# Performance work log

Hardware: AMD Instinct MI355X
Metric: run time of the kernel (lower is better)

The kernel has to match this reference:

```python
import jax, jax.numpy as jnp
import numpy as np

B, LS, LW, LV, M, D, H = 256, 1024, 1024, 1024, 16, 5120, 2048

def setup_inputs() -> dict:
    key = jax.random.key(0)
    ks = jax.random.split(key, 8)
    return {
        'phi_batch': jax.random.normal(ks[0], (B, LS), jnp.float32),
        'w_M_real': jax.random.normal(ks[1], (B, LW, M), jnp.float32),
        'w_M_imag': jax.random.normal(ks[2], (B, LW, M), jnp.float32),
        'v_M': jax.random.normal(ks[3], (LV, M), jnp.float32),
        'W1e': jax.random.normal(ks[4], (D, H), jnp.float32) * 0.02,
        'b1e': jnp.zeros((H,), jnp.float32),
        'W2e': jax.random.normal(ks[5], (H, LS), jnp.float32) * 0.02,
        'b2e': jnp.zeros((LS,), jnp.float32),
        'W1r': jax.random.normal(ks[6], (D, H), jnp.float32) * 0.02,
        'b1r': jnp.zeros((H,), jnp.float32),
        'W2r': jax.random.normal(ks[7], (H, 1), jnp.float32) * 0.02,
        'b2r': jnp.zeros((1,), jnp.float32),
    }

def reference(phi_batch, w_M_real, w_M_imag, v_M, W1e, b1e, W2e, b2e, W1r, b1r, W2r, b2r):
    b, ls = phi_batch.shape
    m = v_M.shape[1]
    # s = (1/sqrt(Ls)) * exp(1j*phi); use real/imag parts directly
    mag = 1.0 / jnp.sqrt(jnp.asarray(ls, jnp.float32))
    s_feat = jnp.concatenate([mag * jnp.cos(phi_batch), mag * jnp.sin(phi_batch)], axis=-1)  # [B, 2Ls]
    # Batched concat across (batch, M): replaces the nested Python loops
    X = jnp.concatenate([
        jnp.broadcast_to(s_feat[:, None, :], (b, m, s_feat.shape[-1])),
        jnp.swapaxes(w_M_real, 1, 2),                       # [B, M, Lw]
        jnp.swapaxes(w_M_imag, 1, 2),                       # [B, M, Lw]
        jnp.broadcast_to(v_M.T[None, :, :], (b, m, v_M.shape[0])),
    ], axis=-1)                                             # [B, M, D]
    eta_M = jax.nn.relu(X @ W1e + b1e) @ W2e + b2e          # [B, M, Ls]
    rho_M = (jax.nn.relu(X @ W1r + b1r) @ W2r + b2r)[..., 0]  # [B, M]
    eta = jnp.einsum('bm,bml->bl', rho_M, eta_M)            # sum_m rho_m * eta_m
    phi_optimal = phi_batch - eta
    return phi_optimal, jnp.swapaxes(eta_M, 1, 2)           # [B, Ls], [B, Ls, M]
```

## Files before the change

kernel.cpp:

```cpp
#include <hip/hip_runtime.h>
#include <hip/hip_bf16.h>
#include <stdint.h>

#define B_    256
#define LS_   1024
#define LW_   1024
#define LV_   1024
#define M_    16
#define D_    5120
#define H_    2048
#define ROWS  4096
#define N1    4096
#define KW    2048

typedef __hip_bfloat16 bf16;
typedef __bf16 bf16x8 __attribute__((ext_vector_type(8)));
typedef __bf16 bf16x4 __attribute__((ext_vector_type(4)));
typedef float f32x4 __attribute__((ext_vector_type(4)));

#define SB0() __builtin_amdgcn_sched_barrier(0)
#define LGKM(n) asm volatile("s_waitcnt lgkmcnt(" #n ")" ::: "memory")
#define VMC(n)  asm volatile("s_waitcnt vmcnt(" #n ")" ::: "memory")

__device__ __forceinline__ void gld_lds16(const void* g, void* l) {
  auto gp = (const __attribute__((address_space(1))) uint32_t*)(uintptr_t)g;
  auto lp = (__attribute__((address_space(3))) uint32_t*)(uint32_t)(uintptr_t)l;
  __builtin_amdgcn_global_load_lds(gp, lp, 16, 0, 0);
}

__device__ __forceinline__ void transpose64_body(char* sm, const float* __restrict__ in,
                                                 bf16* __restrict__ out,
                                                 int C, int R, int r0, int c0, int t) {
  float (*tile)[65] = (float (*)[65])sm;
  const int tx = t & 15, ty = t >> 4;
#pragma unroll
  for (int i = 0; i < 4; ++i) {
    const float4 v = *(const float4*)&in[(size_t)(r0 + ty + i * 16) * C + c0 + tx * 4];
    tile[ty + i * 16][tx * 4 + 0] = v.x;
    tile[ty + i * 16][tx * 4 + 1] = v.y;
    tile[ty + i * 16][tx * 4 + 2] = v.z;
    tile[ty + i * 16][tx * 4 + 3] = v.w;
  }
  __syncthreads();
#pragma unroll
  for (int i = 0; i < 4; ++i) {
    const int n = c0 + ty + i * 16;
    bf16x4 o;
#pragma unroll
    for (int j = 0; j < 4; ++j) o[j] = (__bf16)tile[tx * 4 + j][ty + i * 16];
    *(bf16x4*)&out[(size_t)n * R + r0 + tx * 4] = o;
  }
}

__global__ void __launch_bounds__(256)
prep_kernel(const float* __restrict__ phi,
            const float* __restrict__ wMr, const float* __restrict__ wMi,
            const float* __restrict__ vM,
            const float* __restrict__ W1e, const float* __restrict__ W1r,
            const float* __restrict__ W2e,
            bf16* __restrict__ sfeat, bf16* __restrict__ Awr,
            bf16* __restrict__ W1sT, bf16* __restrict__ W1wT,
            bf16* __restrict__ W2t, float* __restrict__ hVT) {
  __shared__ __align__(16) char sm[32768];
  const int bid = blockIdx.x;
  const int t = threadIdx.x;

  if (bid < 256) {
    float (*vs)[16] = (float (*)[16])sm;
    float (*ws)[16] = (float (*)[16])(sm + 16384);
    const float* Wb = (bid < 128) ? W1e : W1r;
    const int nbase = (bid & 127) * 16;
    const int nout = ((bid < 128) ? 0 : 2048) + nbase;
    const int m = t & 15, nl = t >> 4;
    float acc = 0.f;
    for (int l0 = 0; l0 < 1024; l0 += 256) {
      __syncthreads();
#pragma unroll
      for (int i = 0; i < 16; ++i) {
        int e = i * 256 + t, l = e >> 4, n = e & 15;
        vs[l][n] = vM[(size_t)(l0 + l) * 16 + n];
        ws[l][n] = Wb[(size_t)(4096 + l0 + l) * 2048 + nbase + n];
      }
      __syncthreads();
#pragma unroll 8
      for (int ll = 0; ll < 256; ++ll)
        acc += vs[ll][m] * ws[ll][nl];
    }
    hVT[(size_t)(nout + nl) * 16 + m] = acc;
  } else if (bid < 4352) {
    const int idx = bid - 256;
    const int z = idx >> 10, rem = idx & 1023;
    const float* src = (z == 0 || z == 2) ? W1e : W1r;
    src += (z < 2) ? 0 : (size_t)2048 * 2048;
    bf16* dst = (z < 2) ? W1sT : W1wT;
    dst += (z == 0 || z == 2) ? 0 : (size_t)2048 * 2048;
    transpose64_body(sm, src, dst, 2048, 2048, (rem >> 5) * 64, (rem & 31) * 64, t);
  } else if (bid < 4864) {
    const int idx = bid - 4352;
    transpose64_body(sm, W2e, W2t, LS_, H_, (idx >> 4) * 64, (idx & 15) * 64, t);
  } else if (bid < 8960) {
    const int idx = bid - 4864;
    const int b = idx >> 4, l0 = (idx & 15) * 64;
    float (*tr)[17] = (float (*)[17])sm;
    float (*ti)[17] = (float (*)[17])(sm + 4352 * 4);
    const float* wrb = wMr + (size_t)b * (LW_ * M_) + (size_t)l0 * 16;
    const float* wib = wMi + (size_t)b * (LW_ * M_) + (size_t)l0 * 16;
#pragma unroll
    for (int i = 0; i < 4; ++i) {
      int e = i * 256 + t, l = e >> 4, m = e & 15;
      tr[l][m] = wrb[e];
      ti[l][m] = wib[e];
    }
    __syncthreads();
    int m = t >> 4, t4 = t & 15;
    bf16* outR = Awr + (size_t)(b * 16 + m) * KW + l0;
#pragma unroll
    for (int j = 0; j < 4; ++j) outR[t4 * 4 + j]        = __float2bfloat16(tr[t4 * 4 + j][m]);
#pragma unroll
    for (int j = 0; j < 4; ++j) outR[1024 + t4 * 4 + j] = __float2bfloat16(ti[t4 * 4 + j][m]);
  } else {
    const int i = (bid - 8960) * 256 + t;
    const int b = i >> 10, l = i & 1023;
    float p = phi[i];
    float s, c;
    sincosf(p, &s, &c);
    sfeat[b * 2048 + l]        = __float2bfloat16(0.03125f * c);
    sfeat[b * 2048 + 1024 + l] = __float2bfloat16(0.03125f * s);
  }
}

__global__ void __launch_bounds__(256)
hsum_kernel(const float* __restrict__ hSp, const float* __restrict__ b1e,
            const float* __restrict__ b1r, float* __restrict__ hS2) {
  const int i = (blockIdx.x * 256 + threadIdx.x) * 4;
  const int c = i & (N1 - 1);
  f32x4 v = *(const f32x4*)&hSp[i];
  v = v + *(const f32x4*)&hSp[(size_t)B_ * N1 + i];
  v = v + *(const f32x4*)&hSp[(size_t)2 * B_ * N1 + i];
  v = v + *(const f32x4*)&hSp[(size_t)3 * B_ * N1 + i];
  const float* bp = (c < H_) ? &b1e[c] : &b1r[c - H_];
  v = v + *(const f32x4*)bp;
  *(f32x4*)&hS2[i] = v;
}

__global__ void __launch_bounds__(512, 2)
gemm1_256_kernel(const bf16* __restrict__ A, const bf16* __restrict__ Bt,
                 const float* __restrict__ hS2, const float* __restrict__ hVT,
                 const float* __restrict__ w2r,
                 bf16* __restrict__ outH, float* __restrict__ rhoP) {
  extern __shared__ __align__(16) char smem[];
  constexpr int NT = KW / 32;

  const int tid  = threadIdx.x;
  const int lane = tid & 63;
  const int wave = tid >> 6;
  const int wr = wave >> 2, wc = wave & 3;
  const int fr = lane & 15, fq = lane >> 4;
  const int row0 = blockIdx.y * 256, col0 = blockIdx.x * 256;

  const int slotF = (((fr & 1) << 2) | fq) ^ ((fr >> 1) & 7);
  const int aOff = (wr << 13) + ((fr >> 1) << 7) + (slotF << 4);
  const int bOff = 16384 + (wc << 12) + ((fr >> 1) << 7) + (slotF << 4);

  const int lg0 = (tid >> 3), lg1 = 64 + (tid >> 3);
  const int su0 = (tid & 7) ^ (lg0 & 7), su1 = (tid & 7) ^ (lg1 & 7);
  const int rowp0 = lg0 * 2 + (su0 >> 2), rowp1 = lg1 * 2 + (su1 >> 2);
  const int kb0 = (su0 & 3) << 4, kb1 = (su1 & 3) << 4;
  const char* pA0 = (const char*)A  + (size_t)(row0 + rowp0) * (KW * 2) + kb0;
  const char* pA1 = (const char*)A  + (size_t)(row0 + rowp1) * (KW * 2) + kb1;
  const char* pB0 = (const char*)Bt + (size_t)(col0 + rowp0) * (KW * 2) + kb0;
  const char* pB1 = (const char*)Bt + (size_t)(col0 + rowp1) * (KW * 2) + kb1;

  auto stageTile = [&](int T) {
    char* dst = smem + (size_t)(T & 3) * 32768;
    const size_t ko = (size_t)T * 64;
    gld_lds16(pA0 + ko, dst + 0     + tid * 16);
    gld_lds16(pA1 + ko, dst + 8192  + tid * 16);
    gld_lds16(pB0 + ko, dst + 16384 + tid * 16);
    gld_lds16(pB1 + ko, dst + 24576 + tid * 16);
  };

  f32x4 acc[8][4] = {};
  bf16x8 bA[4], bB[4];

  stageTile(0); stageTile(1); stageTile(2);
  VMC(4);
  __builtin_amdgcn_s_barrier();
  {
    const char* bP = smem + bOff;
#pragma unroll
    for (int n = 0; n < 4; ++n) bA[n] = *(const bf16x8*)(bP + n * 1024);
  }
  SB0();

  auto doIter = [&](int T, bf16x8 (&bCur)[4], bf16x8 (&bNxt)[4]) {
    const char* aP = smem + (size_t)(T & 3) * 32768 + aOff;
    const char* bP = smem + (size_t)((T + 1) & 3) * 32768 + bOff;
    bf16x8 a[8];
#pragma unroll
    for (int m = 0; m < 4; ++m) a[m] = *(const bf16x8*)(aP + m * 1024);
    SB0();
#pragma unroll
    for (int m = 4; m < 8; ++m) a[m] = *(const bf16x8*)(aP + m * 1024);
    SB0();
#pragma unroll
    for (int n = 0; n < 4; ++n) bNxt[n] = *(const bf16x8*)(bP + n * 1024);
    SB0();
    if (T + 3 < NT) stageTile(T + 3);
    SB0();
    LGKM(8);
    SB0();
    __builtin_amdgcn_s_setprio(1);
#pragma unroll
    for (int m = 0; m < 4; ++m)
#pragma unroll
      for (int n = 0; n < 4; ++n)
        acc[m][n] = __builtin_amdgcn_mfma_f32_16x16x32_bf16(a[m], bCur[n], acc[m][n], 0, 0, 0);
    SB0();
    LGKM(4);
    SB0();
#pragma unroll
    for (int m = 4; m < 8; ++m)
#pragma unroll
      for (int n = 0; n < 4; ++n)
        acc[m][n] = __builtin_amdgcn_mfma_f32_16x16x32_bf16(a[m], bCur[n], acc[m][n], 0, 0, 0);
    __builtin_amdgcn_s_setprio(0);
    SB0();
    LGKM(0);
    if (T + 3 < NT) { VMC(4); }
    else            { VMC(0); }
    __builtin_amdgcn_s_barrier();
  };

  for (int t = 0; t < NT - 2; t += 2) {
    doIter(t,     bA, bB);
    doIter(t + 1, bB, bA);
  }
  doIter(NT - 2, bA, bB);

  {
    const char* aP = smem + (size_t)((NT - 1) & 3) * 32768 + aOff;
    bf16x8 a[8];
#pragma unroll
    for (int m = 0; m < 4; ++m) a[m] = *(const bf16x8*)(aP + m * 1024);
    SB0();
#pragma unroll
    for (int m = 4; m < 8; ++m) a[m] = *(const bf16x8*)(aP + m * 1024);
    SB0();
    LGKM(4);
    SB0();
    __builtin_amdgcn_s_setprio(1);
#pragma unroll
    for (int m = 0; m < 4; ++m)
#pragma unroll
      for (int n = 0; n < 4; ++n)
        acc[m][n] = __builtin_amdgcn_mfma_f32_16x16x32_bf16(a[m], bB[n], acc[m][n], 0, 0, 0);
    SB0();
    LGKM(0);
    SB0();
#pragma unroll
    for (int m = 4; m < 8; ++m)
#pragma unroll
      for (int n = 0; n < 4; ++n)
        acc[m][n] = __builtin_amdgcn_mfma_f32_16x16x32_bf16(a[m], bB[n], acc[m][n], 0, 0, 0);
    __builtin_amdgcn_s_setprio(0);
  }

  if (col0 < H_) {
#pragma unroll
    for (int n = 0; n < 4; ++n) {
      const int c = col0 + wc * 64 + n * 16 + fr;
      const f32x4 hv = *(const f32x4*)&hVT[(size_t)c * 16 + fq * 4];
#pragma unroll
      for (int m = 0; m < 8; ++m) {
        const int rbase = row0 + wr * 128 + m * 16;
        const float hs = hS2[(size_t)(rbase >> 4) * N1 + c];
#pragma unroll
        for (int j = 0; j < 4; ++j) {
          const int r = rbase + fq * 4 + j;
          float v = acc[m][n][j] + hs + hv[j];
          outH[(size_t)r * N1 + c] = __float2bfloat16(v > 0.f ? v : 0.f);
        }
      }
    }
  } else {
    const int cb = (col0 >> 8) - 8;
    float* rhoT = (float*)smem;
    f32x4 hv4[4];
    float w2[4];
#pragma unroll
    for (int n = 0; n < 4; ++n) {
      const int c = col0 + wc * 64 + n * 16 + fr;
      hv4[n] = *(const f32x4*)&hVT[(size_t)c * 16 + fq * 4];
      w2[n] = w2r[c - H_];
    }
#pragma unroll
    for (int m = 0; m < 8; ++m) {
      const int rbase = row0 + wr * 128 + m * 16;
      const float* hrow = &hS2[(size_t)(rbase >> 4) * N1];
      f32x4 rsv = {0.f, 0.f, 0.f, 0.f};
#pragma unroll
      for (int n = 0; n < 4; ++n) {
        const int c = col0 + wc * 64 + n * 16 + fr;
        const float hs = hrow[c];
#pragma unroll
        for (int j = 0; j < 4; ++j) {
          float v = acc[m][n][j] + hs + hv4[n][j];
          v = v > 0.f ? v : 0.f;
          rsv[j] += v * w2[n];
        }
      }
#pragma unroll
      for (int j = 0; j < 4; ++j) {
        rsv[j] += __shfl_xor(rsv[j], 1);
        rsv[j] += __shfl_xor(rsv[j], 2);
        rsv[j] += __shfl_xor(rsv[j], 4);
        rsv[j] += __shfl_xor(rsv[j], 8);
      }
      if (fr == 0)
        *(f32x4*)&rhoT[((wr * 4 + wc) << 7) + m * 16 + fq * 4] = rsv;
    }
    __syncthreads();
    if (tid < 256) {
      const int wrr = tid >> 7, lr = tid & 127;
      const float* rt = &rhoT[(wrr * 4) << 7];
      const float s = rt[lr] + rt[128 + lr] + rt[256 + lr] + rt[384 + lr];
      rhoP[(size_t)(row0 + wrr * 128 + lr) * 8 + cb] = s;
    }
  }
}

template <int EPI, int NT>
__global__ void __launch_bounds__(256, 2)
gemm128_pipe_kernel(const bf16* __restrict__ A, int lda,
                    const bf16* __restrict__ Bt, int ldb,
                    const float* __restrict__ bias0,
                    const float* __restrict__ rhoP, const float* __restrict__ b2r,
                    const float* __restrict__ phi,
                    float* __restrict__ outS, float* __restrict__ out0) {
  extern __shared__ __align__(16) char smem[];

  if (EPI == 1) {
    const int z = blockIdx.z;
    A    += (size_t)z * 512;
    Bt   += (size_t)z * 512;
    outS += (size_t)z * ((size_t)B_ * N1);
  }

  const int tid  = threadIdx.x;
  const int lane = tid & 63;
  const int wave = tid >> 6;
  const int wr = wave >> 1, wc = wave & 1;
  const int fr = lane & 15, fq = lane >> 4;
  const int row0 = blockIdx.y * 128, col0 = blockIdx.x * 128;

  if (EPI == 0) {
    if (tid < 128) {
      const float* pp = &rhoP[(size_t)(row0 + tid) * 8];
      const f32x4 p0 = *(const f32x4*)pp;
      const f32x4 p1 = *(const f32x4*)(pp + 4);
      const float s = p0[0] + p0[1] + p0[2] + p0[3] +
                      p1[0] + p1[1] + p1[2] + p1[3] + b2r[0];
      ((float*)(smem + 65536))[tid] = s;
    }
    LGKM(0);
    SB0();
  }

  const int slotF = (((fr & 1) << 2) | fq) ^ ((fr >> 1) & 7);
  const int aOff = (wr << 12) + ((fr >> 1) << 7) + (slotF << 4);
  const int bOff = 8192 + (wc << 12) + ((fr >> 1) << 7) + (slotF << 4);

  const int lgl = tid >> 3;
  const int su  = (tid & 7) ^ (lgl & 7);
  const int rp0 = lgl * 2 + (su >> 2);
  const int rp1 = (32 + lgl) * 2 + (su >> 2);
  const int kb  = (su & 3) << 4;
  const char* pA0 = (const char*)A  + (size_t)(row0 + rp0) * ((size_t)lda * 2) + kb;
  const char* pA1 = (const char*)A  + (size_t)(row0 + rp1) * ((size_t)lda * 2) + kb;
  const char* pB0 = (const char*)Bt + (size_t)(col0 + rp0) * ((size_t)ldb * 2) + kb;
  const char* pB1 = (const char*)Bt + (size_t)(col0 + rp1) * ((size_t)ldb * 2) + kb;

  auto stageTile = [&](int T) {
    char* dst = smem + (size_t)(T & 3) * 16384;
    const size_t ko = (size_t)T * 64;
    gld_lds16(pA0 + ko, dst + 0     + tid * 16);
    gld_lds16(pA1 + ko, dst + 4096  + tid * 16);
    gld_lds16(pB0 + ko, dst + 8192  + tid * 16);
    gld_lds16(pB1 + ko, dst + 12288 + tid * 16);
  };

  f32x4 acc[4][4] = {};
  bf16x8 bA[4], bB[4];

  stageTile(0); stageTile(1); stageTile(2);
  VMC(4);
  __builtin_amdgcn_s_barrier();
  {
    const char* bP = smem + bOff;
#pragma unroll
    for (int n = 0; n < 4; ++n) bA[n] = *(const bf16x8*)(bP + n * 1024);
  }
  SB0();

  auto doIter = [&](int T, bf16x8 (&bCur)[4], bf16x8 (&bNxt)[4]) {
    const char* aP = smem + (size_t)(T & 3) * 16384 + aOff;
    const char* bP = smem + (size_t)((T + 1) & 3) * 16384 + bOff;
    bf16x8 a[4];
#pragma unroll
    for (int m = 0; m < 4; ++m) a[m] = *(const bf16x8*)(aP + m * 1024);
    SB0();
#pragma unroll
    for (int n = 0; n < 4; ++n) bNxt[n] = *(const bf16x8*)(bP + n * 1024);
    SB0();
    if (T + 3 < NT) stageTile(T + 3);
    SB0();
    LGKM(4);
    SB0();
    __builtin_amdgcn_s_setprio(1);
#pragma unroll
    for (int m = 0; m < 4; ++m)
#pragma unroll
      for (int n = 0; n < 4; ++n)
        acc[m][n] = __builtin_amdgcn_mfma_f32_16x16x32_bf16(a[m], bCur[n], acc[m][n], 0, 0, 0);
    __builtin_amdgcn_s_setprio(0);
    SB0();
    LGKM(0);
    if (T + 3 < NT) { VMC(4); }
    else            { VMC(0); }
    __builtin_amdgcn_s_barrier();
  };

  for (int t = 0; t < NT - 2; t += 2) {
    doIter(t,     bA, bB);
    doIter(t + 1, bB, bA);
  }
  doIter(NT - 2, bA, bB);

  {
    const char* aP = smem + (size_t)((NT - 1) & 3) * 16384 + aOff;
    bf16x8 a[4];
#pragma unroll
    for (int m = 0; m < 4; ++m) a[m] = *(const bf16x8*)(aP + m * 1024);
    SB0();
    LGKM(0);
    SB0();
    __builtin_amdgcn_s_setprio(1);
#pragma unroll
    for (int m = 0; m < 4; ++m)
#pragma unroll
      for (int n = 0; n < 4; ++n)
        acc[m][n] = __builtin_amdgcn_mfma_f32_16x16x32_bf16(a[m], bB[n], acc[m][n], 0, 0, 0);
    __builtin_amdgcn_s_setprio(0);
  }

  if (EPI == 0) {
    const float* rhoL = (const float*)(smem + 65536);
#pragma unroll
    for (int m = 0; m < 4; ++m) {
      const int bg = (row0 >> 4) + wr * 4 + m;
      const f32x4 rv = *(const f32x4*)&rhoL[wr * 64 + m * 16 + fq * 4];
#pragma unroll
      for (int n = 0; n < 4; ++n) {
        const int c = col0 + wc * 64 + n * 16 + fr;
        const float bias = bias0[c];
        float part = 0.f;
#pragma unroll
        for (int j = 0; j < 4; ++j) {
          float v = acc[m][n][j] + bias;
          outS[(size_t)bg * (LS_ * M_) + (size_t)c * M_ + (fq * 4 + j)] = v;
          part += rv[j] * v;
        }
        part += __shfl_xor(part, 16);
        part += __shfl_xor(part, 32);
        if (fq == 0)
          out0[(size_t)bg * LS_ + c] = phi[(size_t)bg * LS_ + c] - part;
      }
    }
  } else {
#pragma unroll
    for (int m = 0; m < 4; ++m) {
#pragma unroll
      for (int n = 0; n < 4; ++n) {
        const int c = col0 + wc * 64 + n * 16 + fr;
#pragma unroll
        for (int j = 0; j < 4; ++j) {
          const int r = row0 + wr * 64 + m * 16 + fq * 4 + j;
          outS[(size_t)r * N1 + c] = acc[m][n][j];
        }
      }
    }
  }
}

extern "C" void kernel_launch(void* const* d_in, const int* in_sizes, int n_in,
                              void* d_out, int out_size, void* d_ws, size_t ws_size,
                              hipStream_t stream) {
  const float* phi = (const float*)d_in[0];
  const float* wMr = (const float*)d_in[1];
  const float* wMi = (const float*)d_in[2];
  const float* vM  = (const float*)d_in[3];
  const float* W1e = (const float*)d_in[4];
  const float* b1e = (const float*)d_in[5];
  const float* W2e = (const float*)d_in[6];
  const float* b2e = (const float*)d_in[7];
  const float* W1r = (const float*)d_in[8];
  const float* b1r = (const float*)d_in[9];
  const float* W2r = (const float*)d_in[10];
  const float* b2r = (const float*)d_in[11];

  float* out0 = (float*)d_out;
  float* out1 = out0 + (size_t)B_ * LS_;

  bf16* Awr   = (bf16*)d_ws;
  bf16* W1sT  = Awr  + (size_t)ROWS * KW;
  bf16* W1wT  = W1sT + (size_t)N1 * KW;
  bf16* h     = W1wT + (size_t)N1 * KW;
  bf16* W2t   = h + (size_t)ROWS * N1;
  bf16* sfeat = W2t + (size_t)LS_ * H_;
  float* hSp  = (float*)(sfeat + (size_t)B_ * 2048);
  float* hS2  = hSp + (size_t)4 * B_ * N1;
  float* hVT  = hS2 + (size_t)B_ * N1;
  float* rhoP = hVT + (size_t)N1 * 16;

  (void)hipFuncSetAttribute(reinterpret_cast<const void*>(gemm1_256_kernel),
                            hipFuncAttributeMaxDynamicSharedMemorySize, 131072);
  (void)hipFuncSetAttribute(reinterpret_cast<const void*>(gemm128_pipe_kernel<0, 64>),
                            hipFuncAttributeMaxDynamicSharedMemorySize, 66048);
  (void)hipFuncSetAttribute(reinterpret_cast<const void*>(gemm128_pipe_kernel<1, 16>),
                            hipFuncAttributeMaxDynamicSharedMemorySize, 65536);

  prep_kernel<<<9984, 256, 0, stream>>>(phi, wMr, wMi, vM, W1e, W1r, W2e,
                                        sfeat, Awr, W1sT, W1wT, W2t, hVT);

  gemm128_pipe_kernel<1, 16><<<dim3(N1 / 128, B_ / 128, 4), 256, 65536, stream>>>(
      sfeat, 2048, W1sT, KW, nullptr, nullptr, nullptr, nullptr, hSp, nullptr);

  hsum_kernel<<<(B_ * N1 / 4) / 256, 256, 0, stream>>>(hSp, b1e, b1r, hS2);

  gemm1_256_kernel<<<dim3(N1 / 256, ROWS / 256), 512, 131072, stream>>>(
      Awr, W1wT, hS2, hVT, W2r, h, rhoP);

  gemm128_pipe_kernel<0, 64><<<dim3(LS_ / 128, ROWS / 128), 256, 66048, stream>>>(
      h, N1, W2t, H_, b2e, rhoP, b2r, phi, out1, out0);
}
```

Before: 142.0 us.

## Prefetch next tile's A and B fragments into registers during MFMA

```diff
diff --git a/kernel.cpp b/kernel.cpp
--- a/kernel.cpp
+++ b/kernel.cpp
@@ -181,89 +181,69 @@
   };
 
   f32x4 acc[8][4] = {};
+  bf16x8 a[8];
   bf16x8 bA[4], bB[4];
 
   stageTile(0); stageTile(1); stageTile(2);
   VMC(4);
   __builtin_amdgcn_s_barrier();
   {
-    const char* bP = smem + bOff;
-#pragma unroll
-    for (int n = 0; n < 4; ++n) bA[n] = *(const bf16x8*)(bP + n * 1024);
+    const char* aP0 = smem + aOff;
+    const char* bP0 = smem + bOff;
+#pragma unroll
+    for (int m = 0; m < 4; ++m) a[m] = *(const bf16x8*)(aP0 + m * 1024);
+#pragma unroll
+    for (int n = 0; n < 4; ++n) bA[n] = *(const bf16x8*)(bP0 + n * 1024);
   }
   SB0();
 
   auto doIter = [&](int T, bf16x8 (&bCur)[4], bf16x8 (&bNxt)[4]) {
-    const char* aP = smem + (size_t)(T & 3) * 32768 + aOff;
-    const char* bP = smem + (size_t)((T + 1) & 3) * 32768 + bOff;
-    bf16x8 a[8];
-#pragma unroll
-    for (int m = 0; m < 4; ++m) a[m] = *(const bf16x8*)(aP + m * 1024);
+    const char* aP  = smem + (size_t)(T & 3) * 32768 + aOff;
+    const char* aPn = smem + (size_t)((T + 1) & 3) * 32768 + aOff;
+    const char* bPn = smem + (size_t)((T + 1) & 3) * 32768 + bOff;
+    const bool rb = (T + 1 < NT);
+    const bool pf = (T + 3 < NT);
+
+    LGKM(0);
     SB0();
 #pragma unroll
     for (int m = 4; m < 8; ++m) a[m] = *(const bf16x8*)(aP + m * 1024);
     SB0();
-#pragma unroll
-    for (int n = 0; n < 4; ++n) bNxt[n] = *(const bf16x8*)(bP + n * 1024);
-    SB0();
-    if (T + 3 < NT) stageTile(T + 3);
-    SB0();
-    LGKM(8);
-    SB0();
     __builtin_amdgcn_s_setprio(1);
 #pragma unroll
     for (int m = 0; m < 4; ++m)
-#pragma unroll
-      for (int n = 0; n < 4; ++n)
-        acc[m][n] = __builtin_amdgcn_mfma_f32_16x16x32_bf16(a[m], bCur[n], acc[m][n], 0, 0, 0);
-    SB0();
-    LGKM(4);
-    SB0();
-#pragma unroll
-    for (int m = 4; m < 8; ++m)
 #pragma unroll
       for (int n = 0; n < 4; ++n)
         acc[m][n] = __builtin_amdgcn_mfma_f32_16x16x32_bf16(a[m], bCur[n], acc[m][n], 0, 0, 0);
     __builtin_amdgcn_s_setprio(0);
     SB0();
+
+    if (pf) stageTile(T + 3);
     LGKM(0);
-    if (T + 3 < NT) { VMC(4); }
-    else            { VMC(0); }
+    SB0();
+    if (rb) {
+#pragma unroll
+      for (int m = 0; m < 4; ++m) a[m] = *(const bf16x8*)(aPn + m * 1024);
+#pragma unroll
+      for (int n = 0; n < 4; ++n) bNxt[n] = *(const bf16x8*)(bPn + n * 1024);
+    }
+    SB0();
+    __builtin_amdgcn_s_setprio(1);
+#pragma unroll
+    for (int m = 4; m < 8; ++m)
+#pragma unroll
+      for (int n = 0; n < 4; ++n)
+        acc[m][n] = __builtin_amdgcn_mfma_f32_16x16x32_bf16(a[m], bCur[n], acc[m][n], 0, 0, 0);
+    __builtin_amdgcn_s_setprio(0);
+    SB0();
+    if (pf) { VMC(4); }
+    else    { VMC(0); }
     __builtin_amdgcn_s_barrier();
   };
 
-  for (int t = 0; t < NT - 2; t += 2) {
+  for (int t = 0; t < NT; t += 2) {
     doIter(t,     bA, bB);
     doIter(t + 1, bB, bA);
-  }
-  doIter(NT - 2, bA, bB);
-
-  {
-    const char* aP = smem + (size_t)((NT - 1) & 3) * 32768 + aOff;
-    bf16x8 a[8];
-#pragma unroll
-    for (int m = 0; m < 4; ++m) a[m] = *(const bf16x8*)(aP + m * 1024);
-    SB0();
-#pragma unroll
-    for (int m = 4; m < 8; ++m) a[m] = *(const bf16x8*)(aP + m * 1024);
-    SB0();
-    LGKM(4);
-    SB0();
-    __builtin_amdgcn_s_setprio(1);
-#pragma unroll
-    for (int m = 0; m < 4; ++m)
-#pragma unroll
-      for (int n = 0; n < 4; ++n)
-        acc[m][n] = __builtin_amdgcn_mfma_f32_16x16x32_bf16(a[m], bB[n], acc[m][n], 0, 0, 0);
-    SB0();
-    LGKM(0);
-    SB0();
-#pragma unroll
-    for (int m = 4; m < 8; ++m)
-#pragma unroll
-      for (int n = 0; n < 4; ++n)
-        acc[m][n] = __builtin_amdgcn_mfma_f32_16x16x32_bf16(a[m], bB[n], acc[m][n], 0, 0, 0);
-    __builtin_amdgcn_s_setprio(0);
   }
 
   if (col0 < H_) {
@@ -391,67 +371,54 @@
   };
 
   f32x4 acc[4][4] = {};
-  bf16x8 bA[4], bB[4];
+  bf16x8 aA[4], aB[4], bA[4], bB[4];
 
   stageTile(0); stageTile(1); stageTile(2);
   VMC(4);
   __builtin_amdgcn_s_barrier();
   {
-    const char* bP = smem + bOff;
-#pragma unroll
-    for (int n = 0; n < 4; ++n) bA[n] = *(const bf16x8*)(bP + n * 1024);
+    const char* aP0 = smem + aOff;
+    const char* bP0 = smem + bOff;
+#pragma unroll
+    for (int m = 0; m < 4; ++m) aA[m] = *(const bf16x8*)(aP0 + m * 1024);
+#pragma unroll
+    for (int n = 0; n < 4; ++n) bA[n] = *(const bf16x8*)(bP0 + n * 1024);
   }
   SB0();
 
-  auto doIter = [&](int T, bf16x8 (&bCur)[4], bf16x8 (&bNxt)[4]) {
-    const char* aP = smem + (size_t)(T & 3) * 16384 + aOff;
-    const char* bP = smem + (size_t)((T + 1) & 3) * 16384 + bOff;
-    bf16x8 a[4];
-#pragma unroll
-    for (int m = 0; m < 4; ++m) a[m] = *(const bf16x8*)(aP + m * 1024);
-    SB0();
-#pragma unroll
-    for (int n = 0; n < 4; ++n) bNxt[n] = *(const bf16x8*)(bP + n * 1024);
-    SB0();
-    if (T + 3 < NT) stageTile(T + 3);
-    SB0();
-    LGKM(4);
+  auto doIter = [&](int T, bf16x8 (&aCur)[4], bf16x8 (&bCur)[4],
+                    bf16x8 (&aNxt)[4], bf16x8 (&bNxt)[4]) {
+    const char* aPn = smem + (size_t)((T + 1) & 3) * 16384 + aOff;
+    const char* bPn = smem + (size_t)((T + 1) & 3) * 16384 + bOff;
+    const bool rb = (T + 1 < NT);
+    const bool pf = (T + 3 < NT);
+
+    if (pf) stageTile(T + 3);
+    LGKM(0);
+    SB0();
+    if (rb) {
+#pragma unroll
+      for (int m = 0; m < 4; ++m) aNxt[m] = *(const bf16x8*)(aPn + m * 1024);
+#pragma unroll
+      for (int n = 0; n < 4; ++n) bNxt[n] = *(const bf16x8*)(bPn + n * 1024);
+    }
     SB0();
     __builtin_amdgcn_s_setprio(1);
 #pragma unroll
     for (int m = 0; m < 4; ++m)
 #pragma unroll
       for (int n = 0; n < 4; ++n)
-        acc[m][n] = __builtin_amdgcn_mfma_f32_16x16x32_bf16(a[m], bCur[n], acc[m][n], 0, 0, 0);
+        acc[m][n] = __builtin_amdgcn_mfma_f32_16x16x32_bf16(aCur[m], bCur[n], acc[m][n], 0, 0, 0);
     __builtin_amdgcn_s_setprio(0);
     SB0();
-    LGKM(0);
-    if (T + 3 < NT) { VMC(4); }
-    else            { VMC(0); }
+    if (pf) { VMC(4); }
+    else    { VMC(0); }
     __builtin_amdgcn_s_barrier();
   };
 
-  for (int t = 0; t < NT - 2; t += 2) {
-    doIter(t,     bA, bB);
-    doIter(t + 1, bB, bA);
-  }
-  doIter(NT - 2, bA, bB);
-
-  {
-    const char* aP = smem + (size_t)((NT - 1) & 3) * 16384 + aOff;
-    bf16x8 a[4];
-#pragma unroll
-    for (int m = 0; m < 4; ++m) a[m] = *(const bf16x8*)(aP + m * 1024);
-    SB0();
-    LGKM(0);
-    SB0();
-    __builtin_amdgcn_s_setprio(1);
-#pragma unroll
-    for (int m = 0; m < 4; ++m)
-#pragma unroll
-      for (int n = 0; n < 4; ++n)
-        acc[m][n] = __builtin_amdgcn_mfma_f32_16x16x32_bf16(a[m], bB[n], acc[m][n], 0, 0, 0);
-    __builtin_amdgcn_s_setprio(0);
+  for (int t = 0; t < NT; t += 2) {
+    doIter(t,     aA, bA, aB, bB);
+    doIter(t + 1, aB, bB, aA, bA);
   }
 
   if (EPI == 0) {
```

New measurement: 144.3 us. About the same (+1.6%).
